# Optimization experiments

Measured on AMD Instinct MI355X. Metric: run time of the kernel, lower is better.

Reference implementation:

```python
import jax, jax.numpy as jnp
import numpy as np

B, C, T = 128, 295, 2048
D1 = 270
NUM_SUBJECTS = 64

def setup_inputs() -> dict:
    key = jax.random.key(0)
    k_x, k_s, k_w1, k_b1, k_ws = jax.random.split(key, 5)
    X = jax.random.normal(k_x, (B, C, T), dtype=jnp.float32)
    subject_idxs = jax.random.randint(k_s, (B,), 0, NUM_SUBJECTS)
    W1 = jax.random.normal(k_w1, (D1, C), dtype=jnp.float32) * 0.05
    b1 = jax.random.normal(k_b1, (D1,), dtype=jnp.float32) * 0.05
    Ws = jax.random.normal(k_ws, (NUM_SUBJECTS, D1, D1), dtype=jnp.float32) * 0.05
    return {"X": X, "subject_idxs": subject_idxs, "W1": W1, "b1": b1, "Ws": Ws}

def reference(X, subject_idxs, W1, b1, Ws):
    # Shared 1x1 conv: pointwise channel mix C -> D1 with bias.  [B, D1, T]
    y = jnp.einsum('dc,bct->bdt', W1, X) + b1[None, :, None]
    # Top-1 expert dispatch: gather each sample's subject matrix. [B, D1, D1]
    W_sel = Ws[subject_idxs]
    # Per-sample 1x1 conv (batched GEMM), no bias.            [B, D1, T]
    out = jnp.einsum('bed,bdt->bet', W_sel, y)
    return out
```

## Files before the change

### kernel.cpp

```cpp
#include <hip/hip_runtime.h>
#include <hip/hip_bf16.h>

#define NSUBJ 64
#define CIN   295
#define DD    270
#define TT    2048
#define BB    128

#define WF_PER_S  92160
#define WF_PER_KS 9216
#define W1T_PER_KS 10240

typedef __attribute__((ext_vector_type(8))) short bf16x8;
typedef __attribute__((ext_vector_type(4))) float f32x4;
typedef unsigned short u16;

__device__ __forceinline__ u16 f2bf(float f) {
    return __bfloat16_as_ushort(__float2bfloat16(f));
}

__device__ __forceinline__ void glds16(const void* g, void* lds_base) {
    __builtin_amdgcn_global_load_lds(
        (const __attribute__((address_space(1))) unsigned int*)g,
        (__attribute__((address_space(3))) unsigned int*)lds_base, 16, 0, 0);
}

#define WAITV(N) asm volatile("s_waitcnt vmcnt(" #N ")" ::: "memory")
#define BAR()    __builtin_amdgcn_s_barrier()
#define SB()     __builtin_amdgcn_sched_barrier(0)

__global__ __launch_bounds__(256) void k_prep_w1(const float* __restrict__ W1,
                                                 const float* __restrict__ b1,
                                                 u16* __restrict__ W1t)
{
    const int idx = blockIdx.x * 256 + threadIdx.x;
    const int ks = idx / W1T_PER_KS;
    const int r  = idx - ks * W1T_PER_KS;
    const int kq = r / 2560;
    const int c  = (r - kq * 2560) >> 3;
    const int k8 = r & 7;
    const int d  = ks * 32 + kq * 8 + k8;
    float v = 0.f;
    if (d < DD) {
        if (c < CIN) v = W1[d * CIN + c];
        else if (c == CIN) v = b1[d];
    }
    W1t[idx] = f2bf(v);
}

__global__ __launch_bounds__(256, 1) void k_fuse_w(const float* __restrict__ Ws,
                                                   const u16* __restrict__ W1t,
                                                   u16* __restrict__ Wf)
{
    __shared__ u16 Aw[3072];
    __shared__ u16 Bw[10240];
    const int tid = threadIdx.x, lane = tid & 63, wid = tid >> 6;
    const int wm = wid >> 1, wn = wid & 1;
    const int mt = blockIdx.x, s = blockIdx.y;
    const int e0 = mt * 96;
    const float* Wsb = Ws + (size_t)s * DD * DD;

    f32x4 acc[3][10];
#pragma unroll
    for (int i = 0; i < 3; ++i)
#pragma unroll
        for (int j = 0; j < 10; ++j) acc[i][j] = (f32x4){0.f, 0.f, 0.f, 0.f};

    for (int ks = 0; ks < 9; ++ks) {
        const int k0 = ks * 32;
#pragma unroll
        for (int ci = 0; ci < 3; ++ci) {
            const int id = tid + ci * 256;
            const int m = id >> 3, q = id & 7;
            const int e = e0 + m, d = k0 + q * 4;
            float2 v01 = {0.f, 0.f}, v23 = {0.f, 0.f};
            if (e < DD) {
                if (d < DD)     v01 = *(const float2*)(Wsb + (size_t)e * DD + d);
                if (d + 2 < DD) v23 = *(const float2*)(Wsb + (size_t)e * DD + d + 2);
            }
            ushort4 h;
            h.x = f2bf(v01.x); h.y = f2bf(v01.y); h.z = f2bf(v23.x); h.w = f2bf(v23.y);
            *(ushort4*)(&Aw[(q >> 1) * 768 + m * 8 + (q & 1) * 4]) = h;
        }
#pragma unroll
        for (int k5 = 0; k5 < 5; ++k5) {
            const int seg = wid * 5 + k5;
            glds16(W1t + (size_t)ks * W1T_PER_KS + seg * 512 + lane * 8, &Bw[seg * 512]);
        }
        __syncthreads();
        bf16x8 af[3];
#pragma unroll
        for (int i = 0; i < 3; ++i)
            af[i] = *(const bf16x8*)(&Aw[(lane >> 4) * 768 + (wm * 48 + i * 16 + (lane & 15)) * 8]);
#pragma unroll
        for (int j = 0; j < 10; ++j) {
            const bf16x8 bfj = *(const bf16x8*)(&Bw[(lane >> 4) * 2560 + (wn * 160 + j * 16 + (lane & 15)) * 8]);
#pragma unroll
            for (int i = 0; i < 3; ++i)
                acc[i][j] = __builtin_amdgcn_mfma_f32_16x16x32_bf16(af[i], bfj, acc[i][j], 0, 0, 0);
        }
        __syncthreads();
    }
    const int rb = (lane >> 4) * 4, cc = lane & 15;
#pragma unroll
    for (int i = 0; i < 3; ++i) {
#pragma unroll
        for (int r = 0; r < 4; ++r) {
            const int e = e0 + wm * 48 + i * 16 + rb + r;
#pragma unroll
            for (int j = 0; j < 10; ++j) {
                const int c = wn * 160 + j * 16 + cc;
                Wf[(size_t)s * WF_PER_S + (c >> 5) * WF_PER_KS + ((c >> 3) & 3) * 2304
                   + e * 8 + (c & 7)] = f2bf(acc[i][j][r]);
            }
        }
    }
}

__global__ __launch_bounds__(256, 2) void k_main(const float* __restrict__ X,
                                                 const int* __restrict__ subj,
                                                 const u16* __restrict__ Wf,
                                                 float* __restrict__ out)
{
    __shared__ float Xm[3][2048];
    const int tid = threadIdx.x, lane = tid & 63, wid = tid >> 6;
    const int wm = wid >> 1, wn = wid & 1;
    const int g = lane >> 4, l15 = lane & 15;
    const int hw = blockIdx.x;
    const int w  = (hw & 7) * 512 + (hw >> 3);
    const int b  = w >> 5, nt = w & 31;
    const int t0 = nt * 64;
    const int s = subj[b];
    const float* Xb = X + (size_t)b * CIN * TT;
    const u16* aB = Wf + (size_t)s * WF_PER_S + g * 2304 + (wm * 144 + l15) * 8;

    f32x4 acc[9][2];
#pragma unroll
    for (int i = 0; i < 9; ++i)
#pragma unroll
        for (int j = 0; j < 2; ++j) acc[i][j] = (f32x4){0.f, 0.f, 0.f, 0.f};

#define STAGEX(KS)                                                          \
    {                                                                       \
        _Pragma("unroll")                                                   \
        for (int k2 = 0; k2 < 2; ++k2) {                                    \
            const int seg = wid * 2 + k2;                                   \
            const int cr0 = (KS) * 32 + seg * 4 + g;                        \
            const int cr  = (cr0 < CIN) ? cr0 : (CIN - 1);                  \
            const int sc  = l15 ^ (((seg >> 1) & 3) << 2);                  \
            glds16(Xb + (size_t)cr * TT + t0 + sc * 4,                      \
                   &Xm[(KS) % 3][seg * 256]);                               \
        }                                                                   \
    }
#define COMPUTE(KS, LAST)                                                   \
    {                                                                       \
        bf16x8 af[9];                                                       \
        _Pragma("unroll")                                                   \
        for (int i = 0; i < 9; ++i)                                         \
            af[i] = *(const bf16x8*)(aB + (size_t)(KS) * WF_PER_KS + i * 128);\
        const float* Xc = &Xm[(KS) % 3][0];                                 \
        bf16x8 bfr[2];                                                      \
        _Pragma("unroll")                                                   \
        for (int j = 0; j < 2; ++j) {                                       \
            const int tsw = (wn * 32 + j * 16 + l15) ^ (g << 4);            \
            bf16x8 bb;                                                      \
            _Pragma("unroll")                                               \
            for (int q = 0; q < 8; ++q) {                                   \
                float v = Xc[(g * 8 + q) * 64 + tsw];                       \
                if (LAST) {                                                 \
                    if (q == 7)      v = (g == 0) ? 1.0f : 0.0f;            \
                    else if (g > 0)  v = 0.0f;                              \
                }                                                           \
                bb[q] = (short)f2bf(v);                                     \
            }                                                               \
            bfr[j] = bb;                                                    \
        }                                                                   \
        _Pragma("unroll")                                                   \
        for (int i = 0; i < 9; ++i) {                                       \
            acc[i][0] = __builtin_amdgcn_mfma_f32_16x16x32_bf16(af[i], bfr[0], acc[i][0], 0, 0, 0); \
            acc[i][1] = __builtin_amdgcn_mfma_f32_16x16x32_bf16(af[i], bfr[1], acc[i][1], 0, 0, 0); \
        }                                                                   \
    }

    STAGEX(0); STAGEX(1); SB();
    WAITV(2);
    BAR();

#define STEP(K)                                                             \
    {                                                                       \
        STAGEX((K) + 2); SB();                                              \
        COMPUTE(K, 0);                                                      \
        BAR();                                                              \
    }
    STEP(0) STEP(1) STEP(2) STEP(3) STEP(4) STEP(5) STEP(6) STEP(7)
    COMPUTE(8, 0);
    BAR();
    COMPUTE(9, 1);

    const int rb = g * 4;
#pragma unroll
    for (int i = 0; i < 9; ++i) {
#pragma unroll
        for (int r = 0; r < 4; ++r) {
            const int e = wm * 144 + i * 16 + rb + r;
            if (e < DD) {
#pragma unroll
                for (int j = 0; j < 2; ++j) {
                    const int t = t0 + wn * 32 + j * 16 + l15;
                    out[((size_t)b * DD + e) * TT + t] = acc[i][j][r];
                }
            }
        }
    }
#undef STAGEX
#undef COMPUTE
#undef STEP
}

extern "C" void kernel_launch(void* const* d_in, const int* in_sizes, int n_in,
                              void* d_out, int out_size, void* d_ws, size_t ws_size,
                              hipStream_t stream) {
    const float* X    = (const float*)d_in[0];
    const int*   subj = (const int*)d_in[1];
    const float* W1   = (const float*)d_in[2];
    const float* b1   = (const float*)d_in[3];
    const float* Ws   = (const float*)d_in[4];
    float* out = (float*)d_out;

    u16* Wf  = (u16*)d_ws;
    u16* W1t = (u16*)((char*)d_ws + (size_t)NSUBJ * WF_PER_S * 2);

    k_prep_w1<<<dim3(360), 256, 0, stream>>>(W1, b1, W1t);
    k_fuse_w<<<dim3(3, NSUBJ), 256, 0, stream>>>(Ws, W1t, Wf);
    k_main<<<dim3(TT / 64 * BB), 256, 0, stream>>>(X, subj, Wf, out);
}
```

Before: 206.3 us.

## Give each wave a private X buffer and software-pipeline A loads without barriers

The shared 3-stage X tile, which needed block-wide barriers, becomes per-wave private 4-stage LDS buffers. Each wave now loads only the 32 time columns it consumes, so synchronization reduces to vmcnt waits and s_barrier calls are removed. Weight fragments are double-buffered in registers (even/odd) and prefetched one K-step ahead, hiding global load latency behind MFMA work. In exchange, waves sharing a time half (wn) now each stage the same X rows twice, the prefetched weight fragments add register pressure, and correctness depends on exact vmcnt counts.

```diff
diff --git a/kernel.cpp b/kernel.cpp
--- a/kernel.cpp
+++ b/kernel.cpp
@@ -26,7 +26,6 @@
 }
 
 #define WAITV(N) asm volatile("s_waitcnt vmcnt(" #N ")" ::: "memory")
-#define BAR()    __builtin_amdgcn_s_barrier()
 #define SB()     __builtin_amdgcn_sched_barrier(0)
 
 __global__ __launch_bounds__(256) void k_prep_w1(const float* __restrict__ W1,
@@ -122,7 +121,7 @@
                                                  const u16* __restrict__ Wf,
                                                  float* __restrict__ out)
 {
-    __shared__ float Xm[3][2048];
+    __shared__ float Xp[4][4][1024];
     const int tid = threadIdx.x, lane = tid & 63, wid = tid >> 6;
     const int wm = wid >> 1, wn = wid & 1;
     const int g = lane >> 4, l15 = lane & 15;
@@ -130,9 +129,11 @@
     const int w  = (hw & 7) * 512 + (hw >> 3);
     const int b  = w >> 5, nt = w & 31;
     const int t0 = nt * 64;
+    const int tw0 = t0 + wn * 32;
     const int s = subj[b];
     const float* Xb = X + (size_t)b * CIN * TT;
     const u16* aB = Wf + (size_t)s * WF_PER_S + g * 2304 + (wm * 144 + l15) * 8;
+    float* Xpw = &Xp[wid][0][0];
 
     f32x4 acc[9][2];
 #pragma unroll
@@ -140,33 +141,36 @@
 #pragma unroll
         for (int j = 0; j < 2; ++j) acc[i][j] = (f32x4){0.f, 0.f, 0.f, 0.f};
 
-#define STAGEX(KS)                                                          \
+#define STAGEXP(KS)                                                         \
     {                                                                       \
         _Pragma("unroll")                                                   \
-        for (int k2 = 0; k2 < 2; ++k2) {                                    \
-            const int seg = wid * 2 + k2;                                   \
-            const int cr0 = (KS) * 32 + seg * 4 + g;                        \
+        for (int jj = 0; jj < 4; ++jj) {                                    \
+            const int ct  = jj * 8 + (lane >> 3);                           \
+            const int cr0 = (KS) * 32 + ct;                                 \
             const int cr  = (cr0 < CIN) ? cr0 : (CIN - 1);                  \
-            const int sc  = l15 ^ (((seg >> 1) & 3) << 2);                  \
-            glds16(Xb + (size_t)cr * TT + t0 + sc * 4,                      \
-                   &Xm[(KS) % 3][seg * 256]);                               \
+            const int src = (4 * (lane & 7)) ^ ((jj & 1) << 4);             \
+            glds16(Xb + (size_t)cr * TT + tw0 + src,                        \
+                   Xpw + ((KS) & 3) * 1024 + jj * 256 + (lane & 7) * 4 + (lane >> 3) * 32); \
         }                                                                   \
     }
-#define COMPUTE(KS, LAST)                                                   \
+
+#define LOADA(DST, KS)                                                      \
     {                                                                       \
-        bf16x8 af[9];                                                       \
         _Pragma("unroll")                                                   \
         for (int i = 0; i < 9; ++i)                                         \
-            af[i] = *(const bf16x8*)(aB + (size_t)(KS) * WF_PER_KS + i * 128);\
-        const float* Xc = &Xm[(KS) % 3][0];                                 \
+            DST[i] = *(const bf16x8*)(aB + (size_t)(KS) * WF_PER_KS + i * 128); \
+    }
+#define COMPUTE(KS, AF, LAST)                                               \
+    {                                                                       \
+        const float* Xc = Xpw + ((KS) & 3) * 1024;                          \
         bf16x8 bfr[2];                                                      \
         _Pragma("unroll")                                                   \
         for (int j = 0; j < 2; ++j) {                                       \
-            const int tsw = (wn * 32 + j * 16 + l15) ^ (g << 4);            \
             bf16x8 bb;                                                      \
             _Pragma("unroll")                                               \
             for (int q = 0; q < 8; ++q) {                                   \
-                float v = Xc[(g * 8 + q) * 64 + tsw];                       \
+                const int tsw = (j * 16 + l15) ^ ((g & 1) << 4);            \
+                float v = Xc[(g * 8 + q) * 32 + tsw];                       \
                 if (LAST) {                                                 \
                     if (q == 7)      v = (g == 0) ? 1.0f : 0.0f;            \
                     else if (g > 0)  v = 0.0f;                              \
@@ -177,25 +181,45 @@
         }                                                                   \
         _Pragma("unroll")                                                   \
         for (int i = 0; i < 9; ++i) {                                       \
-            acc[i][0] = __builtin_amdgcn_mfma_f32_16x16x32_bf16(af[i], bfr[0], acc[i][0], 0, 0, 0); \
-            acc[i][1] = __builtin_amdgcn_mfma_f32_16x16x32_bf16(af[i], bfr[1], acc[i][1], 0, 0, 0); \
+            acc[i][0] = __builtin_amdgcn_mfma_f32_16x16x32_bf16(AF[i], bfr[0], acc[i][0], 0, 0, 0); \
+            acc[i][1] = __builtin_amdgcn_mfma_f32_16x16x32_bf16(AF[i], bfr[1], acc[i][1], 0, 0, 0); \
         }                                                                   \
     }
 
-    STAGEX(0); STAGEX(1); SB();
-    WAITV(2);
-    BAR();
-
-#define STEP(K)                                                             \
-    {                                                                       \
-        STAGEX((K) + 2); SB();                                              \
-        COMPUTE(K, 0);                                                      \
-        BAR();                                                              \
-    }
-    STEP(0) STEP(1) STEP(2) STEP(3) STEP(4) STEP(5) STEP(6) STEP(7)
-    COMPUTE(8, 0);
-    BAR();
-    COMPUTE(9, 1);
+    bf16x8 afE[9], afO[9];
+
+    STAGEXP(0);      SB();
+    LOADA(afE, 0);   SB();
+    STAGEXP(1);      SB();
+    STAGEXP(2);      SB();
+
+    LOADA(afO, 1);   SB();
+    STAGEXP(3);      SB();
+    WAITV(21);       SB();
+    COMPUTE(0, afE, 0);
+    LOADA(afE, 2);   SB();
+    STAGEXP(4);      SB();
+    WAITV(17);       SB();
+    COMPUTE(1, afO, 0);
+#define STEP(K, AFL, AFU)                                                   \
+    LOADA(AFL, (K) + 1); SB();                                              \
+    STAGEXP((K) + 3);    SB();                                              \
+    WAITV(17);           SB();                                              \
+    COMPUTE(K, AFU, 0);
+    STEP(2, afO, afE)
+    STEP(3, afE, afO)
+    STEP(4, afO, afE)
+    STEP(5, afE, afO)
+    STEP(6, afO, afE)
+#undef STEP
+    LOADA(afE, 8);   SB();
+    WAITV(13);       SB();
+    COMPUTE(7, afO, 0);
+    LOADA(afO, 9);   SB();
+    WAITV(9);        SB();
+    COMPUTE(8, afE, 0);
+    WAITV(0);        SB();
+    COMPUTE(9, afO, 1);
 
     const int rb = g * 4;
 #pragma unroll
@@ -206,15 +230,15 @@
             if (e < DD) {
 #pragma unroll
                 for (int j = 0; j < 2; ++j) {
-                    const int t = t0 + wn * 32 + j * 16 + l15;
+                    const int t = tw0 + j * 16 + l15;
                     out[((size_t)b * DD + e) * TT + t] = acc[i][j][r];
                 }
             }
         }
     }
-#undef STAGEX
+#undef STAGEXP
+#undef LOADA
 #undef COMPUTE
-#undef STEP
 }
 
 extern "C" void kernel_launch(void* const* d_in, const int* in_sizes, int n_in,
```

Result: slower. 226.4 us (+9.8%).

## Stage fused weights through LDS and split MFMA phases with barriers and priority

Applied to the files above, without the earlier changes.

The fused A-weights are now staged into a triple-buffered LDS array with async global-to-LDS loads, in the same pipeline as the X tiles. Previously each wave read them directly from global memory. Each k-step is split into two half-phases separated by barriers, with the A and X staging interleaved between them, and MFMA bursts are raised in priority via s_setprio. The aim is to hide global latency for the weights and interleave memory traffic with matrix math. The cost is about 55 KB of extra LDS, which may reduce occupancy below the declared 2 blocks per CU, plus more barriers per step.

```diff
diff --git a/kernel.cpp b/kernel.cpp
--- a/kernel.cpp
+++ b/kernel.cpp
@@ -122,6 +122,7 @@
                                                  const u16* __restrict__ Wf,
                                                  float* __restrict__ out)
 {
+    __shared__ u16   Am[3][9216];
     __shared__ float Xm[3][2048];
     const int tid = threadIdx.x, lane = tid & 63, wid = tid >> 6;
     const int wm = wid >> 1, wn = wid & 1;
@@ -132,7 +133,7 @@
     const int t0 = nt * 64;
     const int s = subj[b];
     const float* Xb = X + (size_t)b * CIN * TT;
-    const u16* aB = Wf + (size_t)s * WF_PER_S + g * 2304 + (wm * 144 + l15) * 8;
+    const u16* WfA = Wf + (size_t)s * WF_PER_S;
 
     f32x4 acc[9][2];
 #pragma unroll
@@ -140,6 +141,16 @@
 #pragma unroll
         for (int j = 0; j < 2; ++j) acc[i][j] = (f32x4){0.f, 0.f, 0.f, 0.f};
 
+#define STAGEA(KS)                                                          \
+    {                                                                       \
+        _Pragma("unroll")                                                   \
+        for (int k5 = 0; k5 < 5; ++k5) {                                    \
+            const int seg = wid + 4 * k5;                                   \
+            if (seg < 18)                                                   \
+                glds16(WfA + (size_t)(KS) * WF_PER_KS + seg * 512 + lane * 8,\
+                       &Am[(KS) % 3][seg * 512]);                           \
+        }                                                                   \
+    }
 #define STAGEX(KS)                                                          \
     {                                                                       \
         _Pragma("unroll")                                                   \
@@ -152,50 +163,66 @@
                    &Xm[(KS) % 3][seg * 256]);                               \
         }                                                                   \
     }
-#define COMPUTE(KS, LAST)                                                   \
-    {                                                                       \
-        bf16x8 af[9];                                                       \
+#define WAITSTEP()  { if (wid < 2) WAITV(7); else WAITV(6); }
+#define ENTRY()     { WAITSTEP(); BAR(); SB(); }
+
+#define READA(KS, AF)                                                       \
+    _Pragma("unroll")                                                       \
+    for (int i = 0; i < 9; ++i)                                             \
+        AF[i] = *(const bf16x8*)(&Am[(KS) % 3][g * 2304 + (wm * 144 + i * 16 + l15) * 8]);
+#define BUILDB(KS, J, DST, LAST)                                            \
+    {                                                                       \
+        const float* Xc = &Xm[(KS) % 3][0];                                 \
+        const int tsw = (wn * 32 + (J) * 16 + l15) ^ (g << 4);              \
+        bf16x8 bb;                                                          \
         _Pragma("unroll")                                                   \
-        for (int i = 0; i < 9; ++i)                                         \
-            af[i] = *(const bf16x8*)(aB + (size_t)(KS) * WF_PER_KS + i * 128);\
-        const float* Xc = &Xm[(KS) % 3][0];                                 \
-        bf16x8 bfr[2];                                                      \
-        _Pragma("unroll")                                                   \
-        for (int j = 0; j < 2; ++j) {                                       \
-            const int tsw = (wn * 32 + j * 16 + l15) ^ (g << 4);            \
-            bf16x8 bb;                                                      \
-            _Pragma("unroll")                                               \
-            for (int q = 0; q < 8; ++q) {                                   \
-                float v = Xc[(g * 8 + q) * 64 + tsw];                       \
-                if (LAST) {                                                 \
-                    if (q == 7)      v = (g == 0) ? 1.0f : 0.0f;            \
-                    else if (g > 0)  v = 0.0f;                              \
-                }                                                           \
-                bb[q] = (short)f2bf(v);                                     \
+        for (int q = 0; q < 8; ++q) {                                       \
+            float v = Xc[(g * 8 + q) * 64 + tsw];                           \
+            if (LAST) {                                                     \
+                if (q == 7)      v = (g == 0) ? 1.0f : 0.0f;                \
+                else if (g > 0)  v = 0.0f;                                  \
             }                                                               \
-            bfr[j] = bb;                                                    \
+            bb[q] = (short)f2bf(v);                                         \
         }                                                                   \
-        _Pragma("unroll")                                                   \
-        for (int i = 0; i < 9; ++i) {                                       \
-            acc[i][0] = __builtin_amdgcn_mfma_f32_16x16x32_bf16(af[i], bfr[0], acc[i][0], 0, 0, 0); \
-            acc[i][1] = __builtin_amdgcn_mfma_f32_16x16x32_bf16(af[i], bfr[1], acc[i][1], 0, 0, 0); \
-        }                                                                   \
-    }
-
-    STAGEX(0); STAGEX(1); SB();
-    WAITV(2);
-    BAR();
-
-#define STEP(K)                                                             \
-    {                                                                       \
-        STAGEX((K) + 2); SB();                                              \
-        COMPUTE(K, 0);                                                      \
+        DST = bb;                                                           \
+    }
+#define MFMA9(J, AF, BF)                                                    \
+    __builtin_amdgcn_s_setprio(1);                                          \
+    _Pragma("unroll")                                                       \
+    for (int i = 0; i < 9; ++i)                                             \
+        acc[i][J] = __builtin_amdgcn_mfma_f32_16x16x32_bf16(AF[i], BF, acc[i][J], 0, 0, 0); \
+    __builtin_amdgcn_s_setprio(0);
+
+#define STEP2P(K, STG, LAST)                                                \
+    {                                                                       \
+        bf16x8 af[9], b0, b1;                                               \
+        if (STG) { STAGEA((K) + 2); SB(); }                                 \
+        READA(K, af); BUILDB(K, 0, b0, LAST);                               \
         BAR();                                                              \
-    }
-    STEP(0) STEP(1) STEP(2) STEP(3) STEP(4) STEP(5) STEP(6) STEP(7)
-    COMPUTE(8, 0);
-    BAR();
-    COMPUTE(9, 1);
+        MFMA9(0, af, b0);                                                   \
+        BAR();                                                              \
+        if (STG) { STAGEX((K) + 2); SB(); }                                 \
+        BUILDB(K, 1, b1, LAST);                                             \
+        BAR();                                                              \
+        MFMA9(1, af, b1);                                                   \
+    }
+
+    STAGEA(0); STAGEX(0); SB();
+    STAGEA(1); STAGEX(1); SB();
+    WAITSTEP();
+    BAR(); SB();
+
+    STEP2P(0, 1, 0)
+    ENTRY() STEP2P(1, 1, 0)
+    ENTRY() STEP2P(2, 1, 0)
+    ENTRY() STEP2P(3, 1, 0)
+    ENTRY() STEP2P(4, 1, 0)
+    ENTRY() STEP2P(5, 1, 0)
+    ENTRY() STEP2P(6, 1, 0)
+    ENTRY() STEP2P(7, 1, 0)
+    ENTRY() STEP2P(8, 0, 0)
+    { WAITV(0); BAR(); SB(); }
+    STEP2P(9, 0, 1)
 
     const int rb = g * 4;
 #pragma unroll
@@ -212,9 +239,14 @@
             }
         }
     }
+#undef STAGEA
 #undef STAGEX
-#undef COMPUTE
-#undef STEP
+#undef WAITSTEP
+#undef ENTRY
+#undef READA
+#undef BUILDB
+#undef MFMA9
+#undef STEP2P
 }
 
 extern "C" void kernel_launch(void* const* d_in, const int* in_sizes, int n_in,
```

Result: faster. 194.9 us (-5.5%).
